# Optimization experiments

Measured on AMD Instinct MI355X. Metric: run time of the kernel, lower is better.

The kernel has to match this reference:

```python
import jax, jax.numpy as jnp
import numpy as np

B, T, E = 2, 4096, 768
N_HEADS = 12
HEAD_DIM = E // N_HEADS


def setup_inputs() -> dict:
    key = jax.random.key(0)
    k1, k2, k3 = jax.random.split(key, 3)
    x = jax.random.normal(k1, (B, T, E), dtype=jnp.float32)
    W_attn = jax.random.normal(k2, (E, 3 * E), dtype=jnp.float32) * (1.0 / np.sqrt(E))
    b_attn = jnp.zeros((3 * E,), dtype=jnp.float32)
    W_proj = jax.random.normal(k3, (E, E), dtype=jnp.float32) * (1.0 / np.sqrt(E))
    b_proj = jnp.zeros((E,), dtype=jnp.float32)
    return {"x": x, "W_attn": W_attn, "b_attn": b_attn, "W_proj": W_proj, "b_proj": b_proj}


def reference(x, W_attn, b_attn, W_proj, b_proj):
    Bx, Tx, Ex = x.shape
    qkv = x @ W_attn + b_attn                      # [B,T,3E]
    q, k, v = jnp.split(qkv, 3, axis=-1)
    # [B,T,E] -> [B,H,T,D]
    def to_heads(t):
        return t.reshape(Bx, Tx, N_HEADS, HEAD_DIM).transpose(0, 2, 1, 3)
    q, k, v = to_heads(q), to_heads(k), to_heads(v)
    scale = 1.0 / np.sqrt(HEAD_DIM).astype(np.float32)
    scores = jnp.einsum('bhqd,bhkd->bhqk', q, k) * scale  # [B,H,T,T]
    causal = jnp.tril(jnp.ones((Tx, Tx), dtype=bool))
    scores = jnp.where(causal[None, None, :, :], scores, -jnp.inf)
    probs = jax.nn.softmax(scores, axis=-1)
    y = jnp.einsum('bhqk,bhkd->bhqd', probs, v)    # [B,H,T,D]
    y = y.transpose(0, 2, 1, 3).reshape(Bx, Tx, Ex)
    return y @ W_proj + b_proj
```

## Files before the change

### kernel.cpp

```cpp
#include <hip/hip_runtime.h>


#define SEQT 4096
#define EMB  768
#define NHEAD 12
#define HDIM 64
#define NCHUNK 144

typedef __attribute__((ext_vector_type(8))) short bf16x8;
typedef __attribute__((ext_vector_type(4))) float f32x4;
typedef __attribute__((ext_vector_type(16))) float f32x16;

static __device__ __forceinline__ unsigned short f2bf(float f) {
  union { float f; unsigned u; } a; a.f = f;
  unsigned u = a.u;
  u += 0x7FFF + ((u >> 16) & 1);
  return (unsigned short)(u >> 16);
}

static __device__ __forceinline__ unsigned pack_bf16(float a, float b) {
  union { float f; unsigned u; } ua, ub; ua.f = a; ub.f = b;
  return __builtin_amdgcn_perm(ub.u + 0x8000u, ua.u + 0x8000u, 0x07060302u);
}

static __device__ __forceinline__ void gload_lds16(const short* g, short* l) {
  __builtin_amdgcn_global_load_lds(
      (const __attribute__((address_space(1))) unsigned*)(const void*)g,
      (__attribute__((address_space(3))) unsigned*)(void*)l, 16, 0, 0);
}

__global__ __launch_bounds__(256) void prep_kernel(
    const float* __restrict__ x, short* __restrict__ x_bf,
    const float* __restrict__ W_attn, short* __restrict__ Wt_a,
    const float* __restrict__ W_proj, short* __restrict__ Wt_p) {
  __shared__ float tile[32][33];
  int bid = blockIdx.x;
  int tid = threadIdx.x;
  if (bid < 6144) {
    int i = bid * 256 + tid;
    float4 v = ((const float4*)x)[i];
    ushort4 o;
    o.x = f2bf(v.x); o.y = f2bf(v.y); o.z = f2bf(v.z); o.w = f2bf(v.w);
    ((ushort4*)x_bf)[i] = o;
    return;
  }
  const float* in; short* out; int R, C, c0, r0;
  if (bid < 7872) {
    int t = bid - 6144;
    in = W_attn; out = Wt_a; R = 768; C = 2304;
    c0 = (t % 72) * 32; r0 = (t / 72) * 32;
  } else {
    int t = bid - 7872;
    in = W_proj; out = Wt_p; R = 768; C = 768;
    c0 = (t % 24) * 32; r0 = (t / 24) * 32;
  }
  int tx = tid & 31, ty = tid >> 5;
#pragma unroll
  for (int j = 0; j < 32; j += 8)
    tile[ty + j][tx] = in[(size_t)(r0 + ty + j) * C + (c0 + tx)];
  __syncthreads();
#pragma unroll
  for (int j = 0; j < 32; j += 8)
    out[(size_t)(c0 + ty + j) * R + (r0 + tx)] = (short)f2bf(tile[tx][ty + j]);
}

__global__ __launch_bounds__(256) void gemm_qkv_kernel(
    const short* __restrict__ A, const short* __restrict__ Bt,
    const float* __restrict__ bias, int K,
    short* __restrict__ Qg, short* __restrict__ Kg, short* __restrict__ Vtg) {
  __shared__ short As[128 * 32];
  __shared__ short Bs[128 * 32];
  int tid = threadIdx.x;
  int w = tid >> 6, l = tid & 63, quad = l >> 4, lo = l & 15;
  int wm = (w >> 1) * 64, wn = (w & 1) * 64;
  int gm = blockIdx.x, gn = blockIdx.y;
  f32x4 acc[4][4] = {};
  int c0 = tid, c1 = tid + 256;
  const short* Ag0 = A + (size_t)(gm * 128 + (c0 >> 2)) * K + (c0 & 3) * 8;
  const short* Ag1 = A + (size_t)(gm * 128 + (c1 >> 2)) * K + (c1 & 3) * 8;
  const short* Bg0 = Bt + (size_t)(gn * 128 + (c0 >> 2)) * K + (c0 & 3) * 8;
  const short* Bg1 = Bt + (size_t)(gn * 128 + (c1 >> 2)) * K + (c1 & 3) * 8;

  for (int kk = 0; kk < K; kk += 32) {
    gload_lds16(Ag0 + kk, &As[c0 * 8]);
    gload_lds16(Ag1 + kk, &As[c1 * 8]);
    gload_lds16(Bg0 + kk, &Bs[c0 * 8]);
    gload_lds16(Bg1 + kk, &Bs[c1 * 8]);
    __syncthreads();
    bf16x8 af[4], bf[4];
#pragma unroll
    for (int mt = 0; mt < 4; mt++)
      af[mt] = *(const bf16x8*)&As[(wm + mt * 16 + lo) * 32 + quad * 8];
#pragma unroll
    for (int nt = 0; nt < 4; nt++)
      bf[nt] = *(const bf16x8*)&Bs[(wn + nt * 16 + lo) * 32 + quad * 8];
#pragma unroll
    for (int mt = 0; mt < 4; mt++)
#pragma unroll
      for (int nt = 0; nt < 4; nt++)
        acc[mt][nt] = __builtin_amdgcn_mfma_f32_16x16x32_bf16(bf[nt], af[mt], acc[mt][nt], 0, 0, 0);
    __syncthreads();
  }

#pragma unroll
  for (int nt = 0; nt < 4; nt++) {
    int nb = gn * 128 + wn + nt * 16 + quad * 4;
    float4 bv = *(const float4*)&bias[nb];
#pragma unroll
    for (int mt = 0; mt < 4; mt++) {
      int m = gm * 128 + wm + mt * 16 + lo;
      int b = m >> 12, t = m & 4095;
      float v0 = acc[mt][nt][0] + bv.x;
      float v1 = acc[mt][nt][1] + bv.y;
      float v2 = acc[mt][nt][2] + bv.z;
      float v3 = acc[mt][nt][3] + bv.w;
      if (nb < EMB) {
        int h = nb >> 6, d = nb & 63;
        uint2 u; u.x = pack_bf16(v0, v1); u.y = pack_bf16(v2, v3);
        *(uint2*)&Qg[(((size_t)b * NHEAD + h) * SEQT + t) * HDIM + d] = u;
      } else if (nb < 2 * EMB) {
        int n2 = nb - EMB, h = n2 >> 6, d = n2 & 63;
        uint2 u; u.x = pack_bf16(v0, v1); u.y = pack_bf16(v2, v3);
        *(uint2*)&Kg[(((size_t)b * NHEAD + h) * SEQT + t) * HDIM + d] = u;
      } else {
        int n2 = nb - 2 * EMB, h = n2 >> 6, d = n2 & 63;
        short* vp = &Vtg[(((size_t)b * NHEAD + h) * HDIM + d) * SEQT + t];
        vp[0] = (short)f2bf(v0);
        vp[SEQT] = (short)f2bf(v1);
        vp[2 * SEQT] = (short)f2bf(v2);
        vp[3 * SEQT] = (short)f2bf(v3);
      }
    }
  }
}

__global__ __launch_bounds__(256) void gemm_proj_kernel(
    const short* __restrict__ A, const short* __restrict__ Bt,
    const float* __restrict__ bias, float* __restrict__ Out) {
  __shared__ short As[128 * 32];
  __shared__ short Bs[64 * 32];
  int tid = threadIdx.x;
  int w = tid >> 6, l = tid & 63, quad = l >> 4, lo = l & 15;
  int gm = blockIdx.x, gn = blockIdx.y;
  f32x4 acc[2][4] = {};
  int c0 = tid, c1 = tid + 256;
  const short* Ag0 = A + (size_t)(gm * 128 + (c0 >> 2)) * EMB + (c0 & 3) * 8;
  const short* Ag1 = A + (size_t)(gm * 128 + (c1 >> 2)) * EMB + (c1 & 3) * 8;
  const short* Bg0 = Bt + (size_t)(gn * 64 + (tid >> 2)) * EMB + (tid & 3) * 8;

  for (int kk = 0; kk < EMB; kk += 32) {
    gload_lds16(Ag0 + kk, &As[c0 * 8]);
    gload_lds16(Ag1 + kk, &As[c1 * 8]);
    gload_lds16(Bg0 + kk, &Bs[tid * 8]);
    __syncthreads();
    bf16x8 af[2], bf[4];
#pragma unroll
    for (int mt = 0; mt < 2; mt++)
      af[mt] = *(const bf16x8*)&As[(w * 32 + mt * 16 + lo) * 32 + quad * 8];
#pragma unroll
    for (int nt = 0; nt < 4; nt++)
      bf[nt] = *(const bf16x8*)&Bs[(nt * 16 + lo) * 32 + quad * 8];
#pragma unroll
    for (int mt = 0; mt < 2; mt++)
#pragma unroll
      for (int nt = 0; nt < 4; nt++)
        acc[mt][nt] = __builtin_amdgcn_mfma_f32_16x16x32_bf16(af[mt], bf[nt], acc[mt][nt], 0, 0, 0);
    __syncthreads();
  }

#pragma unroll
  for (int nt = 0; nt < 4; nt++) {
    int n = gn * 64 + nt * 16 + lo;
    float bias_v = bias[n];
#pragma unroll
    for (int mt = 0; mt < 2; mt++) {
#pragma unroll
      for (int r = 0; r < 4; r++) {
        int m = gm * 128 + w * 32 + mt * 16 + quad * 4 + r;
        Out[(size_t)m * EMB + n] = acc[mt][nt][r] + bias_v;
      }
    }
  }
}

#define AP 72
#define VP 136
#define NEG_BIG (-1e9f)
__global__ __launch_bounds__(256, 4) void attn_kernel(
    const short* __restrict__ Qg, const short* __restrict__ Kg,
    const short* __restrict__ Vtg, short* __restrict__ Opart,
    float2* __restrict__ Ml) {
  __shared__ short Ks[128 * AP];
  __shared__ short Vs[64 * VP];
  int tid = threadIdx.x;
  int w = tid >> 6, l = tid & 63;
  int li = l & 31, hi = l >> 5;
  int c = blockIdx.x;
  int bh = blockIdx.y;
  int qt = 31, rem = c;
  while (rem >= ((qt + 4) >> 2)) { rem -= (qt + 4) >> 2; qt--; }
  int p = rem;
  int q0 = qt * 128;
  int cid = bh * NCHUNK + c;
  const short* Qbase = Qg + (size_t)bh * SEQT * HDIM;
  const short* Kbase = Kg + (size_t)bh * SEQT * HDIM;
  const short* Vbase = Vtg + (size_t)bh * HDIM * SEQT;

  int qw = q0 + w * 32;
  bf16x8 qf[4];
#pragma unroll
  for (int kk = 0; kk < 4; kk++)
    qf[kk] = *(const bf16x8*)&Qbase[(size_t)(qw + li) * HDIM + kk * 16 + hi * 8];

  f32x16 O[2] = {};
  float m_s = NEG_BIG;
  float l_s = 0.f;

  int kr = tid >> 1, kc = tid & 1;
  int vr = tid >> 2, vc = tid & 3;
  const float SC = 0.18033688011112042f;
  int s_begin = 4 * p;
  int s_end = min(4 * p + 4, qt + 1);

  for (int s = s_begin; s < s_end; s++) {
    int kv0 = s * 128;
    {
      const short* kg = &Kbase[(size_t)(kv0 + kr) * HDIM + kc * 32];
      uint4 a0 = ((const uint4*)kg)[0];
      uint4 a1 = ((const uint4*)kg)[1];
      uint4 a2 = ((const uint4*)kg)[2];
      uint4 a3 = ((const uint4*)kg)[3];
      short* kd = &Ks[kr * AP + kc * 32];
      ((uint4*)kd)[0] = a0; ((uint4*)kd)[1] = a1;
      ((uint4*)kd)[2] = a2; ((uint4*)kd)[3] = a3;
    }
    {
      const short* vg = &Vbase[(size_t)vr * SEQT + kv0 + vc * 32];
      uint4 b0 = ((const uint4*)vg)[0];
      uint4 b1 = ((const uint4*)vg)[1];
      uint4 b2 = ((const uint4*)vg)[2];
      uint4 b3 = ((const uint4*)vg)[3];
      short* vd = &Vs[vr * VP + vc * 32];
      ((uint4*)vd)[0] = b0; ((uint4*)vd)[1] = b1;
      ((uint4*)vd)[2] = b2; ((uint4*)vd)[3] = b3;
    }
    __syncthreads();

#pragma unroll
    for (int h2 = 0; h2 < 2; h2++) {
      int kvh = kv0 + h2 * 64;
      if (kvh > qw) break;
      bool act1 = (kvh + 32 <= qw);
      bf16x8 ka0[4], ka1[4];
#pragma unroll
      for (int kk = 0; kk < 4; kk++)
        ka0[kk] = *(const bf16x8*)&Ks[(h2 * 64 + li) * AP + kk * 16 + hi * 8];
      if (act1) {
#pragma unroll
        for (int kk = 0; kk < 4; kk++)
          ka1[kk] = *(const bf16x8*)&Ks[(h2 * 64 + 32 + li) * AP + kk * 16 + hi * 8];
      }

      f32x16 st[2];
      {
        f32x16 a = {};
#pragma unroll
        for (int kk = 0; kk < 4; kk++)
          a = __builtin_amdgcn_mfma_f32_32x32x16_bf16(ka0[kk], qf[kk], a, 0, 0, 0);
        st[0] = a;
      }
      if (act1) {
        f32x16 a = {};
#pragma unroll
        for (int kk = 0; kk < 4; kk++)
          a = __builtin_amdgcn_mfma_f32_32x32x16_bf16(ka1[kk], qf[kk], a, 0, 0, 0);
        st[1] = a;
      }

      bool full0 = (kvh < qw);
      float mx = NEG_BIG;
      if (full0) {
#pragma unroll
        for (int r = 0; r < 16; r++) mx = fmaxf(mx, st[0][r]);
      } else {
        int thr = li - 4 * hi;
#pragma unroll
        for (int r = 0; r < 16; r++) {
          const int R = (r & 3) + 8 * (r >> 2);
          st[0][r] = (R <= thr) ? st[0][r] : NEG_BIG;
          mx = fmaxf(mx, st[0][r]);
        }
      }
      if (act1) {
        bool full1 = (kvh + 32 < qw);
        if (full1) {
#pragma unroll
          for (int r = 0; r < 16; r++) mx = fmaxf(mx, st[1][r]);
        } else {
          int thr = li - 4 * hi;
#pragma unroll
          for (int r = 0; r < 16; r++) {
            const int R = (r & 3) + 8 * (r >> 2);
            st[1][r] = (R <= thr) ? st[1][r] : NEG_BIG;
            mx = fmaxf(mx, st[1][r]);
          }
        }
      }
      mx = fmaxf(mx, __shfl_xor(mx, 32));
      float mn = fmaxf(m_s, mx);
      float c1 = SC * mn;
      float al = __builtin_amdgcn_exp2f(fminf(SC * m_s - c1, 0.f));
      m_s = mn;
      float sm = 0.f;
      unsigned pk[2][8];
#pragma unroll
      for (int r2 = 0; r2 < 8; r2++) {
        float pa = __builtin_amdgcn_exp2f(fminf(__builtin_fmaf(st[0][2 * r2],     SC, -c1), 0.f));
        float pb = __builtin_amdgcn_exp2f(fminf(__builtin_fmaf(st[0][2 * r2 + 1], SC, -c1), 0.f));
        sm += pa + pb;
        pk[0][r2] = pack_bf16(pa, pb);
      }
      if (act1) {
#pragma unroll
        for (int r2 = 0; r2 < 8; r2++) {
          float pa = __builtin_amdgcn_exp2f(fminf(__builtin_fmaf(st[1][2 * r2],     SC, -c1), 0.f));
          float pb = __builtin_amdgcn_exp2f(fminf(__builtin_fmaf(st[1][2 * r2 + 1], SC, -c1), 0.f));
          sm += pa + pb;
          pk[1][r2] = pack_bf16(pa, pb);
        }
      }
      sm += __shfl_xor(sm, 32);
      l_s = l_s * al + sm;
#pragma unroll
      for (int dt = 0; dt < 2; dt++)
#pragma unroll
        for (int r = 0; r < 16; r++) O[dt][r] *= al;

#pragma unroll
      for (int g = 0; g < 4; g++) {
        int t = g >> 1, k2 = g & 1;
        if (t == 1 && !act1) continue;
        unsigned own_a = hi ? pk[t][k2 * 4 + 2] : pk[t][k2 * 4 + 0];
        unsigned own_b = hi ? pk[t][k2 * 4 + 3] : pk[t][k2 * 4 + 1];
        unsigned snd_a = hi ? pk[t][k2 * 4 + 0] : pk[t][k2 * 4 + 2];
        unsigned snd_b = hi ? pk[t][k2 * 4 + 1] : pk[t][k2 * 4 + 3];
        unsigned rcv_a = (unsigned)__shfl_xor((int)snd_a, 32);
        unsigned rcv_b = (unsigned)__shfl_xor((int)snd_b, 32);
        union { unsigned u[4]; bf16x8 v; } pf;
        pf.u[0] = hi ? rcv_a : own_a;
        pf.u[1] = hi ? rcv_b : own_b;
        pf.u[2] = hi ? own_a : rcv_a;
        pf.u[3] = hi ? own_b : rcv_b;
        bf16x8 va0 = *(const bf16x8*)&Vs[li * VP + h2 * 64 + g * 16 + hi * 8];
        bf16x8 va1 = *(const bf16x8*)&Vs[(32 + li) * VP + h2 * 64 + g * 16 + hi * 8];
        O[0] = __builtin_amdgcn_mfma_f32_32x32x16_bf16(va0, pf.v, O[0], 0, 0, 0);
        O[1] = __builtin_amdgcn_mfma_f32_32x32x16_bf16(va1, pf.v, O[1], 0, 0, 0);
      }
    }
    __syncthreads();
  }

  int lq = w * 32 + li;
  short* op = &Opart[((size_t)cid * 128 + lq) * 64];
#pragma unroll
  for (int dt = 0; dt < 2; dt++) {
#pragma unroll
    for (int rg = 0; rg < 4; rg++) {
      uint2 u2;
      u2.x = pack_bf16(O[dt][rg * 4 + 0], O[dt][rg * 4 + 1]);
      u2.y = pack_bf16(O[dt][rg * 4 + 2], O[dt][rg * 4 + 3]);
      *(uint2*)(op + dt * 32 + rg * 8 + hi * 4) = u2;
    }
  }
  if (hi == 0) {
    float2 ml; ml.x = m_s; ml.y = l_s;
    Ml[(size_t)cid * 128 + lq] = ml;
  }
}

__global__ __launch_bounds__(256) void merge_kernel(
    const short* __restrict__ Opart, const float2* __restrict__ Ml,
    short* __restrict__ Y) {
  int qt = blockIdx.x, bh = blockIdx.y;
  int n = (qt + 4) >> 2;
  int cbase = 0;
  for (int j = qt + 1; j < 32; j++) cbase += (j + 4) >> 2;
  int tid = threadIdx.x;
  int lq = tid >> 1, half = tid & 1;
  int b = bh / NHEAD, h = bh % NHEAD;
  int q = qt * 128 + lq;
  const float SC = 0.18033688011112042f;

  float m_i[8], l_i[8];
  float mstar = NEG_BIG;
#pragma unroll 4
  for (int i = 0; i < n; i++) {
    float2 ml = Ml[((size_t)bh * NCHUNK + cbase + i) * 128 + lq];
    m_i[i] = ml.x; l_i[i] = ml.y;
    mstar = fmaxf(mstar, ml.x);
  }
  float lstar = 0.f;
  float wgt[8];
#pragma unroll 4
  for (int i = 0; i < n; i++) {
    wgt[i] = __builtin_amdgcn_exp2f(fminf(SC * (m_i[i] - mstar), 0.f));
    lstar += l_i[i] * wgt[i];
  }

  float acc[32] = {};
#pragma unroll 4
  for (int i = 0; i < n; i++) {
    const short* op = &Opart[(((size_t)bh * NCHUNK + cbase + i) * 128 + lq) * 64 + half * 32];
    float wi = wgt[i];
#pragma unroll
    for (int v = 0; v < 4; v++) {
      uint4 u = ((const uint4*)op)[v];
      unsigned uu[4] = {u.x, u.y, u.z, u.w};
#pragma unroll
      for (int j = 0; j < 4; j++) {
        union { unsigned u; float f; } lo2, hi2;
        lo2.u = uu[j] << 16;
        hi2.u = uu[j] & 0xFFFF0000u;
        acc[v * 8 + j * 2]     = __builtin_fmaf(lo2.f, wi, acc[v * 8 + j * 2]);
        acc[v * 8 + j * 2 + 1] = __builtin_fmaf(hi2.f, wi, acc[v * 8 + j * 2 + 1]);
      }
    }
  }
  float rl = 1.f / lstar;
  short* yp = &Y[((size_t)b * SEQT + q) * EMB + h * 64 + half * 32];
#pragma unroll
  for (int v = 0; v < 4; v++) {
    uint2 u2;
    u2.x = pack_bf16(acc[v * 8 + 0] * rl, acc[v * 8 + 1] * rl);
    u2.y = pack_bf16(acc[v * 8 + 2] * rl, acc[v * 8 + 3] * rl);
    uint2 u3;
    u3.x = pack_bf16(acc[v * 8 + 4] * rl, acc[v * 8 + 5] * rl);
    u3.y = pack_bf16(acc[v * 8 + 6] * rl, acc[v * 8 + 7] * rl);
    *(uint2*)(yp + v * 8) = u2;
    *(uint2*)(yp + v * 8 + 4) = u3;
  }
}

extern "C" void kernel_launch(void* const* d_in, const int* in_sizes, int n_in,
                              void* d_out, int out_size, void* d_ws, size_t ws_size,
                              hipStream_t stream) {
  const float* x      = (const float*)d_in[0];
  const float* W_attn = (const float*)d_in[1];
  const float* b_attn = (const float*)d_in[2];
  const float* W_proj = (const float*)d_in[3];
  const float* b_proj = (const float*)d_in[4];
  float* out = (float*)d_out;

  char* ws = (char*)d_ws;
  short* x_bf  = (short*)(ws + 0);
  short* Wt_a  = (short*)(ws + 12582912);
  short* Wt_p  = (short*)(ws + 16121856);
  short* Qg    = (short*)(ws + 17301504);
  short* Kg    = (short*)(ws + 29884416);
  short* Vtg   = (short*)(ws + 42467328);
  short* Ybf   = (short*)(ws + 55050240);
  short* Opart = (short*)(ws + 67633152);
  float2* Ml   = (float2*)(ws + 124256256);

  prep_kernel<<<8448, 256, 0, stream>>>(x, x_bf, W_attn, Wt_a, W_proj, Wt_p);

  gemm_qkv_kernel<<<dim3(64, 18), 256, 0, stream>>>(x_bf, Wt_a, b_attn, 768,
                                                    Qg, Kg, Vtg);
  attn_kernel<<<dim3(NCHUNK, 24), 256, 0, stream>>>(Qg, Kg, Vtg, Opart, Ml);
  merge_kernel<<<dim3(32, 24), 256, 0, stream>>>(Opart, Ml, Ybf);
  gemm_proj_kernel<<<dim3(64, 12), 256, 0, stream>>>(Ybf, Wt_p, b_proj, out);
}
```

Baseline: 278.4 us.

## Rewrite QKV GEMM as 256x256 double-buffered 8-wave kernel with interleaved prefetch

Replaces the 128x128 single-buffered QKV GEMM with a 512-thread, 256x256-tile kernel using BK=64 and double-buffered LDS. Global-to-LDS prefetches for the next k-step are spread between four MFMA phases, and s_setprio is raised around the MFMA blocks. This targets the load latency and barrier stalls of the old loop and raises reuse per tile. In exchange it uses 128KB of LDS per block and launches only 288 blocks, which may underfill the GPU.

```diff
diff --git a/kernel.cpp b/kernel.cpp
--- a/kernel.cpp
+++ b/kernel.cpp
@@ -64,52 +64,144 @@
     out[(size_t)(c0 + ty + j) * R + (r0 + tx)] = (short)f2bf(tile[tx][ty + j]);
 }
 
-__global__ __launch_bounds__(256) void gemm_qkv_kernel(
+__global__ __launch_bounds__(512, 2) void gemm_qkv8_kernel(
     const short* __restrict__ A, const short* __restrict__ Bt,
-    const float* __restrict__ bias, int K,
+    const float* __restrict__ bias,
     short* __restrict__ Qg, short* __restrict__ Kg, short* __restrict__ Vtg) {
-  __shared__ short As[128 * 32];
-  __shared__ short Bs[128 * 32];
+  __shared__ short As[2][256 * 64];
+  __shared__ short Bs[2][256 * 64];
   int tid = threadIdx.x;
   int w = tid >> 6, l = tid & 63, quad = l >> 4, lo = l & 15;
-  int wm = (w >> 1) * 64, wn = (w & 1) * 64;
+  int wm = (w >> 2) * 128, wn = (w & 3) * 64;
   int gm = blockIdx.x, gn = blockIdx.y;
-  f32x4 acc[4][4] = {};
-  int c0 = tid, c1 = tid + 256;
-  const short* Ag0 = A + (size_t)(gm * 128 + (c0 >> 2)) * K + (c0 & 3) * 8;
-  const short* Ag1 = A + (size_t)(gm * 128 + (c1 >> 2)) * K + (c1 & 3) * 8;
-  const short* Bg0 = Bt + (size_t)(gn * 128 + (c0 >> 2)) * K + (c0 & 3) * 8;
-  const short* Bg1 = Bt + (size_t)(gn * 128 + (c1 >> 2)) * K + (c1 & 3) * 8;
-
-  for (int kk = 0; kk < K; kk += 32) {
-    gload_lds16(Ag0 + kk, &As[c0 * 8]);
-    gload_lds16(Ag1 + kk, &As[c1 * 8]);
-    gload_lds16(Bg0 + kk, &Bs[c0 * 8]);
-    gload_lds16(Bg1 + kk, &Bs[c1 * 8]);
-    __syncthreads();
-    bf16x8 af[4], bf[4];
+  f32x4 acc[8][4] = {};
+
+  const short* Ag = A  + (size_t)(gm * 256 + (l >> 3)) * 768 + (l & 7) * 8;
+  const short* Bg = Bt + (size_t)(gn * 256 + (l >> 3)) * 768 + (l & 7) * 8;
+  const int lds_off = w * 2048 + l * 8;
+
+#pragma unroll
+  for (int j = 0; j < 4; j++) {
+    gload_lds16(Ag + (size_t)(w * 4 + j) * 8 * 768, &As[0][lds_off + j * 512]);
+    gload_lds16(Bg + (size_t)(w * 4 + j) * 8 * 768, &Bs[0][lds_off + j * 512]);
+  }
+  asm volatile("s_waitcnt vmcnt(0)" ::: "memory");
+  __builtin_amdgcn_s_barrier();
+
+#pragma unroll 1
+  for (int t = 0; t < 12; t++) {
+    const int c = t & 1;
+    const short* Ac = As[c];
+    const short* Bc = Bs[c];
+    short* An = (short*)As[c ^ 1];
+    short* Bn = (short*)Bs[c ^ 1];
+    const bool pf = (t + 1 < 12);
+    const int kn = (t + 1) * 64;
+
+    bf16x8 af[4][2], bf[2][2];
+
+    if (pf) {
+      gload_lds16(Ag + (size_t)(w * 4 + 0) * 8 * 768 + kn, &An[lds_off + 0 * 512]);
+      gload_lds16(Ag + (size_t)(w * 4 + 1) * 8 * 768 + kn, &An[lds_off + 1 * 512]);
+      gload_lds16(Ag + (size_t)(w * 4 + 2) * 8 * 768 + kn, &An[lds_off + 2 * 512]);
+    }
 #pragma unroll
     for (int mt = 0; mt < 4; mt++)
-      af[mt] = *(const bf16x8*)&As[(wm + mt * 16 + lo) * 32 + quad * 8];
-#pragma unroll
-    for (int nt = 0; nt < 4; nt++)
-      bf[nt] = *(const bf16x8*)&Bs[(wn + nt * 16 + lo) * 32 + quad * 8];
+#pragma unroll
+      for (int ks = 0; ks < 2; ks++)
+        af[mt][ks] = *(const bf16x8*)&Ac[(wm + mt * 16 + lo) * 64 + ks * 32 + quad * 8];
+#pragma unroll
+    for (int nt = 0; nt < 2; nt++)
+#pragma unroll
+      for (int ks = 0; ks < 2; ks++)
+        bf[nt][ks] = *(const bf16x8*)&Bc[(wn + nt * 16 + lo) * 64 + ks * 32 + quad * 8];
+    __builtin_amdgcn_s_barrier();
+    __builtin_amdgcn_s_setprio(1);
 #pragma unroll
     for (int mt = 0; mt < 4; mt++)
 #pragma unroll
-      for (int nt = 0; nt < 4; nt++)
-        acc[mt][nt] = __builtin_amdgcn_mfma_f32_16x16x32_bf16(bf[nt], af[mt], acc[mt][nt], 0, 0, 0);
-    __syncthreads();
+      for (int nt = 0; nt < 2; nt++)
+#pragma unroll
+        for (int ks = 0; ks < 2; ks++)
+          acc[mt][nt] = __builtin_amdgcn_mfma_f32_16x16x32_bf16(bf[nt][ks], af[mt][ks], acc[mt][nt], 0, 0, 0);
+    __builtin_amdgcn_s_setprio(0);
+    __builtin_amdgcn_s_barrier();
+
+    if (pf) {
+      gload_lds16(Ag + (size_t)(w * 4 + 3) * 8 * 768 + kn, &An[lds_off + 3 * 512]);
+      gload_lds16(Bg + (size_t)(w * 4 + 0) * 8 * 768 + kn, &Bn[lds_off + 0 * 512]);
+      gload_lds16(Bg + (size_t)(w * 4 + 1) * 8 * 768 + kn, &Bn[lds_off + 1 * 512]);
+    }
+#pragma unroll
+    for (int nt = 0; nt < 2; nt++)
+#pragma unroll
+      for (int ks = 0; ks < 2; ks++)
+        bf[nt][ks] = *(const bf16x8*)&Bc[(wn + (2 + nt) * 16 + lo) * 64 + ks * 32 + quad * 8];
+    __builtin_amdgcn_s_barrier();
+    __builtin_amdgcn_s_setprio(1);
+#pragma unroll
+    for (int mt = 0; mt < 4; mt++)
+#pragma unroll
+      for (int nt = 0; nt < 2; nt++)
+#pragma unroll
+        for (int ks = 0; ks < 2; ks++)
+          acc[mt][2 + nt] = __builtin_amdgcn_mfma_f32_16x16x32_bf16(bf[nt][ks], af[mt][ks], acc[mt][2 + nt], 0, 0, 0);
+    __builtin_amdgcn_s_setprio(0);
+    __builtin_amdgcn_s_barrier();
+
+    if (pf) {
+      gload_lds16(Bg + (size_t)(w * 4 + 2) * 8 * 768 + kn, &Bn[lds_off + 2 * 512]);
+      gload_lds16(Bg + (size_t)(w * 4 + 3) * 8 * 768 + kn, &Bn[lds_off + 3 * 512]);
+    }
+#pragma unroll
+    for (int mt = 0; mt < 4; mt++)
+#pragma unroll
+      for (int ks = 0; ks < 2; ks++)
+        af[mt][ks] = *(const bf16x8*)&Ac[(wm + (4 + mt) * 16 + lo) * 64 + ks * 32 + quad * 8];
+#pragma unroll
+    for (int nt = 0; nt < 2; nt++)
+#pragma unroll
+      for (int ks = 0; ks < 2; ks++)
+        bf[nt][ks] = *(const bf16x8*)&Bc[(wn + nt * 16 + lo) * 64 + ks * 32 + quad * 8];
+    __builtin_amdgcn_s_barrier();
+    __builtin_amdgcn_s_setprio(1);
+#pragma unroll
+    for (int mt = 0; mt < 4; mt++)
+#pragma unroll
+      for (int nt = 0; nt < 2; nt++)
+#pragma unroll
+        for (int ks = 0; ks < 2; ks++)
+          acc[4 + mt][nt] = __builtin_amdgcn_mfma_f32_16x16x32_bf16(bf[nt][ks], af[mt][ks], acc[4 + mt][nt], 0, 0, 0);
+    __builtin_amdgcn_s_setprio(0);
+    __builtin_amdgcn_s_barrier();
+
+#pragma unroll
+    for (int nt = 0; nt < 2; nt++)
+#pragma unroll
+      for (int ks = 0; ks < 2; ks++)
+        bf[nt][ks] = *(const bf16x8*)&Bc[(wn + (2 + nt) * 16 + lo) * 64 + ks * 32 + quad * 8];
+    asm volatile("s_waitcnt vmcnt(0)" ::: "memory");
+    __builtin_amdgcn_s_barrier();
+    __builtin_amdgcn_s_setprio(1);
+#pragma unroll
+    for (int mt = 0; mt < 4; mt++)
+#pragma unroll
+      for (int nt = 0; nt < 2; nt++)
+#pragma unroll
+        for (int ks = 0; ks < 2; ks++)
+          acc[4 + mt][2 + nt] = __builtin_amdgcn_mfma_f32_16x16x32_bf16(bf[nt][ks], af[mt][ks], acc[4 + mt][2 + nt], 0, 0, 0);
+    __builtin_amdgcn_s_setprio(0);
+    __builtin_amdgcn_s_barrier();
   }
 
 #pragma unroll
   for (int nt = 0; nt < 4; nt++) {
-    int nb = gn * 128 + wn + nt * 16 + quad * 4;
+    int nb = gn * 256 + wn + nt * 16 + quad * 4;
     float4 bv = *(const float4*)&bias[nb];
 #pragma unroll
-    for (int mt = 0; mt < 4; mt++) {
-      int m = gm * 128 + wm + mt * 16 + lo;
-      int b = m >> 12, t = m & 4095;
+    for (int mt = 0; mt < 8; mt++) {
+      int m = gm * 256 + wm + mt * 16 + lo;
+      int b = m >> 12, tt = m & 4095;
       float v0 = acc[mt][nt][0] + bv.x;
       float v1 = acc[mt][nt][1] + bv.y;
       float v2 = acc[mt][nt][2] + bv.z;
@@ -117,14 +209,14 @@
       if (nb < EMB) {
         int h = nb >> 6, d = nb & 63;
         uint2 u; u.x = pack_bf16(v0, v1); u.y = pack_bf16(v2, v3);
-        *(uint2*)&Qg[(((size_t)b * NHEAD + h) * SEQT + t) * HDIM + d] = u;
+        *(uint2*)&Qg[(((size_t)b * NHEAD + h) * SEQT + tt) * HDIM + d] = u;
       } else if (nb < 2 * EMB) {
         int n2 = nb - EMB, h = n2 >> 6, d = n2 & 63;
         uint2 u; u.x = pack_bf16(v0, v1); u.y = pack_bf16(v2, v3);
-        *(uint2*)&Kg[(((size_t)b * NHEAD + h) * SEQT + t) * HDIM + d] = u;
+        *(uint2*)&Kg[(((size_t)b * NHEAD + h) * SEQT + tt) * HDIM + d] = u;
       } else {
         int n2 = nb - 2 * EMB, h = n2 >> 6, d = n2 & 63;
-        short* vp = &Vtg[(((size_t)b * NHEAD + h) * HDIM + d) * SEQT + t];
+        short* vp = &Vtg[(((size_t)b * NHEAD + h) * HDIM + d) * SEQT + tt];
         vp[0] = (short)f2bf(v0);
         vp[SEQT] = (short)f2bf(v1);
         vp[2 * SEQT] = (short)f2bf(v2);
@@ -464,7 +556,7 @@
 
   prep_kernel<<<8448, 256, 0, stream>>>(x, x_bf, W_attn, Wt_a, W_proj, Wt_p);
 
-  gemm_qkv_kernel<<<dim3(64, 18), 256, 0, stream>>>(x_bf, Wt_a, b_attn, 768,
+  gemm_qkv8_kernel<<<dim3(32, 9), 512, 0, stream>>>(x_bf, Wt_a, b_attn,
                                                     Qg, Kg, Vtg);
   attn_kernel<<<dim3(NCHUNK, 24), 256, 0, stream>>>(Qg, Kg, Vtg, Opart, Ml);
   merge_kernel<<<dim3(32, 24), 256, 0, stream>>>(Opart, Ml, Ybf);
```

After: 326.8 us. 1.17x slower.
